# Performance work log

Hardware: AMD Instinct MI355X
Metric: run time of the kernel (lower is better)

The kernel has to match this reference:

```python
import jax, jax.numpy as jnp
import numpy as np

D = 1024
N_HEAD = 16
D_HEAD = D // N_HEAD
B, S = 4, 2048
EPS = 1e-6


def rmsnorm(x, w):
    # x: [..., d_head]
    return x / jnp.sqrt(jnp.mean(x * x, axis=-1, keepdims=True) + EPS) * w


def setup_inputs() -> dict:
    key = jax.random.key(0)
    ks = jax.random.split(key, 6)
    x = jax.random.normal(ks[0], (B, S, D), dtype=jnp.float32)
    # causal mask: True means masked (upper triangle above diagonal)
    mask = jnp.triu(jnp.ones((S, S), dtype=bool), k=1)
    scale = 1.0 / np.sqrt(D)
    W_qkv = jax.random.normal(ks[1], (D, 3 * D), dtype=jnp.float32) * scale
    b_qkv = jnp.zeros((3 * D,), dtype=jnp.float32)
    W_o = jax.random.normal(ks[2], (D, D), dtype=jnp.float32) * scale
    b_o = jnp.zeros((D,), dtype=jnp.float32)
    wq = jnp.ones((D_HEAD,), dtype=jnp.float32)
    wk = jnp.ones((D_HEAD,), dtype=jnp.float32)
    return {"x": x, "mask": mask, "W_qkv": W_qkv, "b_qkv": b_qkv,
            "W_o": W_o, "b_o": b_o, "wq": wq, "wk": wk}


def reference(x, mask, W_qkv, b_qkv, W_o, b_o, wq, wk):
    b, s, d = x.shape
    qkv = x @ W_qkv + b_qkv  # [b,s,3d]
    q, k, v = jnp.split(qkv, 3, axis=-1)
    q = q.reshape(b, s, N_HEAD, D_HEAD)
    k = k.reshape(b, s, N_HEAD, D_HEAD)
    v = v.reshape(b, s, N_HEAD, D_HEAD)
    q = rmsnorm(q, wq)
    k = rmsnorm(k, wk)
    # NOTE: no 1/sqrt(d_head) scaling, faithful to the source
    attn = jnp.einsum('bqhd,bkhd->bhqk', q, k)
    attn = jnp.where(mask[None, None, :, :], -jnp.inf, attn)
    attn = jax.nn.softmax(attn, axis=-1)
    z = jnp.einsum('bhqk,bkhd->bqhd', attn, v).reshape(b, s, d)
    return z @ W_o + b_o
```

## Files before the change

### kernel.cpp

```cpp
#include <hip/hip_runtime.h>
#include <cmath>

typedef _Float16 half_t;
typedef _Float16 half8 __attribute__((ext_vector_type(8)));
typedef _Float16 half4v __attribute__((ext_vector_type(4)));
typedef float float4v __attribute__((ext_vector_type(4)));

#define LOG2E 1.44269504088896340736f

#define GLDS16(g, l)                                                                   \
    __builtin_amdgcn_global_load_lds((const __attribute__((address_space(1))) void*)(g), \
                                     (__attribute__((address_space(3))) void*)(l), 16, 0, 0)

#define BAR_LGKM() __asm__ volatile("s_waitcnt lgkmcnt(0)\n\ts_barrier" ::: "memory")
#define BAR_VM(n)  __asm__ volatile("s_waitcnt vmcnt(" #n ")\n\ts_barrier" ::: "memory")

__global__ void cast_f32_f16(const float* __restrict__ in, half_t* __restrict__ out, int n) {
    int i = (blockIdx.x * blockDim.x + threadIdx.x) * 4;
    if (i >= n) return;
    float4 v = *(const float4*)(in + i);
    half4v o;
    o[0] = (half_t)v.x; o[1] = (half_t)v.y; o[2] = (half_t)v.z; o[3] = (half_t)v.w;
    *(half4v*)(out + i) = o;
}

__global__ void transpose_cast(const float* __restrict__ in, half_t* __restrict__ out, int R, int C) {
    __shared__ float tile[32][33];
    int c0 = blockIdx.x * 32, r0 = blockIdx.y * 32;
    int tx = threadIdx.x, ty = threadIdx.y;
    for (int p = 0; p < 4; p++) {
        int r = r0 + ty + p * 8;
        tile[ty + p * 8][tx] = in[(size_t)r * C + c0 + tx];
    }
    __syncthreads();
    for (int p = 0; p < 4; p++) {
        int c = c0 + ty + p * 8;
        out[(size_t)c * R + r0 + tx] = (half_t)tile[tx][ty + p * 8];
    }
}

template <int MODE>
__global__ __launch_bounds__(256) void gemm_f16(
    const half_t* __restrict__ A,
    const half_t* __restrict__ Bt,
    const float* __restrict__ bias,
    void* __restrict__ Cout,
    int M, int N, int K,
    const float* __restrict__ wq, const float* __restrict__ wk,
    half_t* __restrict__ Qh, half_t* __restrict__ Kh)
{
    __shared__ __align__(16) half_t As[2][128 * 32];
    __shared__ __align__(16) half_t Bs[2][128 * 32];
    int t = threadIdx.x;
    int lane = t & 63, w = t >> 6;
    int m0 = blockIdx.x * 128, n0 = blockIdx.y * 128;
    int wm = (w >> 1) * 64, wn = (w & 1) * 64;
    int lrow = lane & 15, quad = lane >> 4;

    const half_t* gA = A  + (size_t)(m0 + (t >> 2)) * K + (t & 3) * 8;
    const half_t* gB = Bt + (size_t)(n0 + (t >> 2)) * K + (t & 3) * 8;
    half_t* ldsA[2] = { &As[0][w * 512], &As[1][w * 512] };
    half_t* ldsB[2] = { &Bs[0][w * 512], &Bs[1][w * 512] };

    float4v acc[4][4] = {};

    GLDS16(gA,                  ldsA[0]);
    GLDS16(gA + (size_t)64 * K, ldsA[0] + 2048);
    GLDS16(gB,                  ldsB[0]);
    GLDS16(gB + (size_t)64 * K, ldsB[0] + 2048);

    int nk = K >> 5;
    for (int ki = 0; ki < nk; ki++) {
        int cur = ki & 1, nxt = cur ^ 1;
        int k0 = ki << 5;
        BAR_LGKM();
        if (ki + 1 < nk) {
            GLDS16(gA + k0 + 32,                  ldsA[nxt]);
            GLDS16(gA + (size_t)64 * K + k0 + 32, ldsA[nxt] + 2048);
            GLDS16(gB + k0 + 32,                  ldsB[nxt]);
            GLDS16(gB + (size_t)64 * K + k0 + 32, ldsB[nxt] + 2048);
            BAR_VM(4);
        } else {
            BAR_VM(0);
        }
        half8 af[4], bf[4];
        for (int i = 0; i < 4; i++) af[i] = *(const half8*)(&As[cur][(wm + i * 16 + lrow) * 32 + quad * 8]);
        for (int i = 0; i < 4; i++) bf[i] = *(const half8*)(&Bs[cur][(wn + i * 16 + lrow) * 32 + quad * 8]);
        for (int mi = 0; mi < 4; mi++)
            for (int ni = 0; ni < 4; ni++)
                acc[mi][ni] = __builtin_amdgcn_mfma_f32_16x16x32_f16(af[mi], bf[ni], acc[mi][ni], 0, 0, 0);
    }

    if (MODE == 0) {
        float* out = (float*)Cout;
        for (int mi = 0; mi < 4; mi++)
            for (int ni = 0; ni < 4; ni++)
                for (int r = 0; r < 4; r++) {
                    int gr = m0 + wm + mi * 16 + quad * 4 + r;
                    int gc = n0 + wn + ni * 16 + lrow;
                    out[(size_t)gr * N + gc] = acc[mi][ni][r] + bias[gc];
                }
    } else {
        int nglob = n0 + wn;
        if (nglob < 2048) {
            int isK = nglob >> 10;
            int h = (nglob >> 6) & 15;
            const float* wv = isK ? wk : wq;
            half_t* dst = isK ? Kh : Qh;
            float post = isK ? 1.0f : LOG2E;
            for (int mi = 0; mi < 4; mi++)
                for (int r = 0; r < 4; r++) {
                    int gr = m0 + wm + mi * 16 + quad * 4 + r;
                    float v[4]; float ss = 0.f;
                    for (int ni = 0; ni < 4; ni++) {
                        v[ni] = acc[mi][ni][r] + bias[nglob + ni * 16 + lrow];
                        ss += v[ni] * v[ni];
                    }
                    ss += __shfl_xor(ss, 1);
                    ss += __shfl_xor(ss, 2);
                    ss += __shfl_xor(ss, 4);
                    ss += __shfl_xor(ss, 8);
                    float rr = rsqrtf(ss * (1.0f / 64.0f) + 1e-6f) * post;
                    int bb = gr >> 11, s = gr & 2047;
                    size_t rowbase = ((size_t)((bb * 16 + h) * 2048 + s)) * 64;
                    for (int ni = 0; ni < 4; ni++) {
                        int d = ni * 16 + lrow;
                        dst[rowbase + d] = (half_t)(v[ni] * rr * wv[d]);
                    }
                }
        } else {
            half_t* Vt = (half_t*)Cout;
            for (int mi = 0; mi < 4; mi++) {
                int gr = m0 + wm + mi * 16 + quad * 4;
                int bb = gr >> 11, s = gr & 2047;
                for (int ni = 0; ni < 4; ni++) {
                    int dg = nglob + ni * 16 + lrow - 2048;
                    float bv = bias[nglob + ni * 16 + lrow];
                    half4v oh;
                    for (int r = 0; r < 4; r++) oh[r] = (half_t)(acc[mi][ni][r] + bv);
                    *(half4v*)(Vt + ((size_t)((bb * 16 + (dg >> 6)) * 64 + (dg & 63))) * 2048 + s) = oh;
                }
            }
        }
    }
}

__global__ __launch_bounds__(512, 4) void attn(
    const half_t* __restrict__ Qh, const half_t* __restrict__ Kh, const half_t* __restrict__ Vt,
    half_t* __restrict__ Z)
{
    __shared__ __align__(16) half_t Ks[2][64 * 64];
    __shared__ __align__(16) half_t Vs[2][64 * 64];
    __shared__ __align__(16) half_t Ps[8 * 16 * 64];

    int bh = blockIdx.x;
    int b = bh >> 4, h = bh & 15;
    int t = threadIdx.x, lane = t & 63, w = t >> 6;
    int lrow = lane & 15, quad = lane >> 4;

    int sr = w * 8 + (lane >> 3);
    int scc = (lane & 7) ^ ((lane >> 3) & 7);
    const half_t* gK0 = Kh + ((size_t)bh * 2048 + sr) * 64 + scc * 8;
    const half_t* gV0 = Vt + ((size_t)bh * 64 + sr) * 2048 + scc * 8;

    int sw = lrow & 7;
    int cA = (quad ^ sw) * 8;
    int cB = ((quad + 4) ^ sw) * 8;
    half_t* PsW = Ps + w * 1024 + lrow * 64;

    for (int pass = 0; pass < 2; pass++) {
        int qt = pass ? (15 - (int)blockIdx.y) : (int)blockIdx.y;
        int q0w = qt * 128 + w * 16;

        const half_t* Qbase = Qh + ((size_t)bh * 2048 + q0w + lrow) * 64;
        half8 qf0 = *(const half8*)(Qbase + quad * 8);
        half8 qf1 = *(const half8*)(Qbase + 32 + quad * 8);

        float4v ot[4] = {};
        float m = -__builtin_inff(), l = 0.f;

        int nt = 2 * qt + 2;
        __syncthreads();
        GLDS16(gK0, &Ks[0][w * 512]);
        GLDS16(gV0, &Vs[0][w * 512]);

        for (int kt = 0; kt < nt; kt++) {
            int cur = kt & 1, nxt = cur ^ 1;
            int kb = kt * 64;
            BAR_LGKM();
            if (kt + 1 < nt) {
                GLDS16(gK0 + (size_t)(kb + 64) * 64, &Ks[nxt][w * 512]);
                GLDS16(gV0 + kb + 64,                &Vs[nxt][w * 512]);
                BAR_VM(2);
            } else {
                BAR_VM(0);
            }
            if (kb > q0w + 15) continue;

            float4v st[4];
            for (int f = 0; f < 4; f++) {
                float4v z = {};
                const half_t* kr = &Ks[cur][(f * 16 + lrow) * 64];
                half8 k0 = *(const half8*)(kr + cA);
                half8 k1 = *(const half8*)(kr + cB);
                z = __builtin_amdgcn_mfma_f32_16x16x32_f16(k0, qf0, z, 0, 0, 0);
                z = __builtin_amdgcn_mfma_f32_16x16x32_f16(k1, qf1, z, 0, 0, 0);
                st[f] = z;
            }
            if (kb + 63 > q0w) {
                int qabs = q0w + lrow;
                for (int f = 0; f < 4; f++)
                    for (int r = 0; r < 4; r++) {
                        int key = kb + f * 16 + quad * 4 + r;
                        if (key > qabs) st[f][r] = -__builtin_inff();
                    }
            }
            float tm = st[0][0];
            for (int f = 0; f < 4; f++)
                for (int r = 0; r < 4; r++) tm = fmaxf(tm, st[f][r]);
            tm = fmaxf(tm, __shfl_xor(tm, 16));
            tm = fmaxf(tm, __shfl_xor(tm, 32));
            float mn = fmaxf(m, tm);
            float alpha = __builtin_amdgcn_exp2f(m - mn);
            m = mn;
            float rs = 0.f;
            for (int f = 0; f < 4; f++) {
                float p0 = __builtin_amdgcn_exp2f(st[f][0] - mn);
                float p1 = __builtin_amdgcn_exp2f(st[f][1] - mn);
                float p2 = __builtin_amdgcn_exp2f(st[f][2] - mn);
                float p3 = __builtin_amdgcn_exp2f(st[f][3] - mn);
                rs += (p0 + p1) + (p2 + p3);
                uint2 pw;
                pw.x = __builtin_bit_cast(unsigned, __builtin_amdgcn_cvt_pkrtz(p0, p1));
                pw.y = __builtin_bit_cast(unsigned, __builtin_amdgcn_cvt_pkrtz(p2, p3));
                int cc = (2 * f + (quad >> 1)) ^ sw;
                *(uint2*)(PsW + cc * 8 + (quad & 1) * 4) = pw;
            }
            rs += __shfl_xor(rs, 16);
            rs += __shfl_xor(rs, 32);
            l = l * alpha + rs;
            for (int f2 = 0; f2 < 4; f2++)
                for (int r = 0; r < 4; r++) ot[f2][r] *= alpha;

            __asm__ volatile("s_waitcnt lgkmcnt(0)" ::: "memory");
            half8 p0v = *(const half8*)(PsW + cA);
            half8 p1v = *(const half8*)(PsW + cB);
            for (int f2 = 0; f2 < 4; f2++) {
                const half_t* vr = &Vs[cur][(f2 * 16 + lrow) * 64];
                half8 v0 = *(const half8*)(vr + cA);
                half8 v1 = *(const half8*)(vr + cB);
                ot[f2] = __builtin_amdgcn_mfma_f32_16x16x32_f16(v0, p0v, ot[f2], 0, 0, 0);
                ot[f2] = __builtin_amdgcn_mfma_f32_16x16x32_f16(v1, p1v, ot[f2], 0, 0, 0);
            }
        }

        float inv = 1.0f / l;
        size_t base = ((size_t)(b * 2048) + q0w + lrow) * 1024 + h * 64;
        for (int f2 = 0; f2 < 4; f2++) {
            half4v oh;
            for (int r = 0; r < 4; r++) oh[r] = (half_t)(ot[f2][r] * inv);
            *(half4v*)(Z + base + f2 * 16 + quad * 4) = oh;
        }
    }
}

extern "C" void kernel_launch(void* const* d_in, const int* in_sizes, int n_in,
                              void* d_out, int out_size, void* d_ws, size_t ws_size,
                              hipStream_t stream)
{
    const float* x     = (const float*)d_in[0];
    const float* W_qkv = (const float*)d_in[2];
    const float* b_qkv = (const float*)d_in[3];
    const float* W_o   = (const float*)d_in[4];
    const float* b_o   = (const float*)d_in[5];
    const float* wq    = (const float*)d_in[6];
    const float* wk    = (const float*)d_in[7];
    float* out = (float*)d_out;

    char* ws = (char*)d_ws;
    half_t* xh   = (half_t*)(ws);
    half_t* Wqt  = (half_t*)(ws + (16ull << 20));
    half_t* Wot  = (half_t*)(ws + (22ull << 20));
    half_t* Qh   = (half_t*)(ws + (40ull << 20));
    half_t* Kh   = (half_t*)(ws + (56ull << 20));
    half_t* Vt   = (half_t*)(ws + (72ull << 20));
    half_t* zh   = xh;

    cast_f32_f16<<<8192, 256, 0, stream>>>(x, xh, 8192 * 1024);
    transpose_cast<<<dim3(96, 32), dim3(32, 8), 0, stream>>>(W_qkv, Wqt, 1024, 3072);
    transpose_cast<<<dim3(32, 32), dim3(32, 8), 0, stream>>>(W_o, Wot, 1024, 1024);
    gemm_f16<1><<<dim3(64, 24), 256, 0, stream>>>(xh, Wqt, b_qkv, Vt, 8192, 3072, 1024,
                                                  wq, wk, Qh, Kh);
    attn<<<dim3(64, 8), 512, 0, stream>>>(Qh, Kh, Vt, zh);
    gemm_f16<0><<<dim3(64, 8), 256, 0, stream>>>(zh, Wot, b_o, out, 8192, 1024, 1024,
                                                 nullptr, nullptr, nullptr, nullptr);
}
```

Measured before the change: 284.7 us.

## Triple-buffer GEMM LDS tiles and swizzle K-chunks to avoid bank conflicts

Moves the f16 GEMM's LDS staging from double to triple buffering, prefetching two K-steps ahead with matching vmcnt waits, so global-to-LDS loads overlap more MFMA work. It also rotates the 8-element K-chunk position per row, both when writing via global_load_lds and when reading fragments, to spread ds_read accesses across LDS banks. LDS use grows to 48KB per block, which may reduce occupancy.

```diff
diff --git a/kernel.cpp b/kernel.cpp
--- a/kernel.cpp
+++ b/kernel.cpp
@@ -49,43 +49,52 @@
     const float* __restrict__ wq, const float* __restrict__ wk,
     half_t* __restrict__ Qh, half_t* __restrict__ Kh)
 {
-    __shared__ __align__(16) half_t As[2][128 * 32];
-    __shared__ __align__(16) half_t Bs[2][128 * 32];
+    __shared__ __align__(16) half_t As[3][128 * 32];
+    __shared__ __align__(16) half_t Bs[3][128 * 32];
     int t = threadIdx.x;
     int lane = t & 63, w = t >> 6;
     int m0 = blockIdx.x * 128, n0 = blockIdx.y * 128;
     int wm = (w >> 1) * 64, wn = (w & 1) * 64;
     int lrow = lane & 15, quad = lane >> 4;
 
-    const half_t* gA = A  + (size_t)(m0 + (t >> 2)) * K + (t & 3) * 8;
-    const half_t* gB = Bt + (size_t)(n0 + (t >> 2)) * K + (t & 3) * 8;
-    half_t* ldsA[2] = { &As[0][w * 512], &As[1][w * 512] };
-    half_t* ldsB[2] = { &Bs[0][w * 512], &Bs[1][w * 512] };
+    int lc = ((t & 3) - (t >> 3)) & 3;
+    const half_t* gA = A  + (size_t)(m0 + (t >> 2)) * K + lc * 8;
+    const half_t* gB = Bt + (size_t)(n0 + (t >> 2)) * K + lc * 8;
+    half_t* ldsA[3] = { &As[0][w * 512], &As[1][w * 512], &As[2][w * 512] };
+    half_t* ldsB[3] = { &Bs[0][w * 512], &Bs[1][w * 512], &Bs[2][w * 512] };
+
+    int posq = (quad + (lrow >> 1)) & 3;
 
     float4v acc[4][4] = {};
 
-    GLDS16(gA,                  ldsA[0]);
-    GLDS16(gA + (size_t)64 * K, ldsA[0] + 2048);
-    GLDS16(gB,                  ldsB[0]);
-    GLDS16(gB + (size_t)64 * K, ldsB[0] + 2048);
+    GLDS16(gA,                       ldsA[0]);
+    GLDS16(gA + (size_t)64 * K,      ldsA[0] + 2048);
+    GLDS16(gB,                       ldsB[0]);
+    GLDS16(gB + (size_t)64 * K,      ldsB[0] + 2048);
+    GLDS16(gA + 32,                  ldsA[1]);
+    GLDS16(gA + (size_t)64 * K + 32, ldsA[1] + 2048);
+    GLDS16(gB + 32,                  ldsB[1]);
+    GLDS16(gB + (size_t)64 * K + 32, ldsB[1] + 2048);
 
     int nk = K >> 5;
     for (int ki = 0; ki < nk; ki++) {
-        int cur = ki & 1, nxt = cur ^ 1;
-        int k0 = ki << 5;
+        int cur = ki % 3, pre = (ki + 2) % 3;
         BAR_LGKM();
-        if (ki + 1 < nk) {
-            GLDS16(gA + k0 + 32,                  ldsA[nxt]);
-            GLDS16(gA + (size_t)64 * K + k0 + 32, ldsA[nxt] + 2048);
-            GLDS16(gB + k0 + 32,                  ldsB[nxt]);
-            GLDS16(gB + (size_t)64 * K + k0 + 32, ldsB[nxt] + 2048);
+        if (ki + 2 < nk) {
+            int kp = (ki + 2) << 5;
+            GLDS16(gA + kp,                  ldsA[pre]);
+            GLDS16(gA + (size_t)64 * K + kp, ldsA[pre] + 2048);
+            GLDS16(gB + kp,                  ldsB[pre]);
+            GLDS16(gB + (size_t)64 * K + kp, ldsB[pre] + 2048);
+            BAR_VM(8);
+        } else if (ki + 1 < nk) {
             BAR_VM(4);
         } else {
             BAR_VM(0);
         }
         half8 af[4], bf[4];
-        for (int i = 0; i < 4; i++) af[i] = *(const half8*)(&As[cur][(wm + i * 16 + lrow) * 32 + quad * 8]);
-        for (int i = 0; i < 4; i++) bf[i] = *(const half8*)(&Bs[cur][(wn + i * 16 + lrow) * 32 + quad * 8]);
+        for (int i = 0; i < 4; i++) af[i] = *(const half8*)(&As[cur][(wm + i * 16 + lrow) * 32 + posq * 8]);
+        for (int i = 0; i < 4; i++) bf[i] = *(const half8*)(&Bs[cur][(wn + i * 16 + lrow) * 32 + posq * 8]);
         for (int mi = 0; mi < 4; mi++)
             for (int ni = 0; ni < 4; ni++)
                 acc[mi][ni] = __builtin_amdgcn_mfma_f32_16x16x32_f16(af[mi], bf[ni], acc[mi][ni], 0, 0, 0);
```

Measured after the change: 286.3 us. About the same (+0.6%).
